# Kernel tuning notes

Hardware: AMD Instinct MI355X
Metric: run time of the kernel (lower is better)

The kernel has to match this reference:

```python
import math
import jax, jax.numpy as jnp
import numpy as np

R2PI = math.sqrt(2.0 * math.pi)


def setup_inputs() -> dict:
    key = jax.random.key(0)
    k1, k2, k3 = jax.random.split(key, 3)
    B, N, D = 16, 1024, 512
    feats = jax.random.normal(k1, (B, N, D), dtype=jnp.float32)
    ranges = jax.random.uniform(k2, (B, N), dtype=jnp.float32)  # Gaussian stddev per token
    durations = jax.random.randint(k3, (B, N), 1, 8, dtype=jnp.int64)
    # outlen is data-dependent in the torch code (.item()); fix it here as a static int
    outlen = int(jnp.max(jnp.sum(durations, axis=1)))
    return {"feats": feats, "ranges": ranges, "durations": durations, "outlen": outlen}


def reference(feats, ranges, durations, outlen):
    # feats: (B, N, D); ranges, durations: (B, N); outlen: static int
    dur = durations.astype(jnp.float32)
    # center per token (faithful to source: dur/2 + inclusive cumsum)
    c = dur / 2.0 + jnp.cumsum(dur, axis=1)            # (B, N)
    r = ranges + 1e-6                                   # (B, N)
    t = jnp.arange(outlen, dtype=jnp.float32)           # (T,)
    # z[b, t, n] = (t - c[b, n]) / r[b, n]
    z = (t[None, :, None] - c[:, None, :]) / r[:, None, :]          # (B, T, N)
    weights = jnp.exp(-0.5 * z * z) / (r[:, None, :] * R2PI) + 1e-6  # (B, T, N)
    weights = weights / jnp.sum(weights, axis=2, keepdims=True)
    # weighted sum of phoneme features per output frame
    return jnp.einsum("btn,bnd->btd", weights, feats)   # (B, T, D)
```

## Files before the change

kernel.cpp:

```cpp
#include <hip/hip_runtime.h>
#include <math.h>


#define B_ 16
#define N_ 1024
#define D_ 512
#define TB 8
#define MAXW 36
#define NCH 32

__global__ void scan_k(const int* __restrict__ dur, float* __restrict__ Q,
                       float* __restrict__ C) {
    int b = blockIdx.x;
    int lane = threadIdx.x;
    const int PER = N_ / 64;
    int base = b * N_ + lane * PER;
    int loc[PER];
    int s = 0;
#pragma unroll
    for (int i = 0; i < PER; ++i) { loc[i] = dur[base + i]; s += loc[i]; }
    int x = s;
#pragma unroll
    for (int off = 1; off < 64; off <<= 1) {
        int y = __shfl_up(x, off);
        if (lane >= off) x += y;
    }
    int run = x - s;
#pragma unroll
    for (int i = 0; i < PER; ++i) {
        Q[base + i] = (float)run;
        C[base + i] = (float)run + 1.5f * (float)loc[i];
        run += loc[i];
    }
}

__global__ void sumP_k(const float* __restrict__ feats, float* __restrict__ P) {
    int b = blockIdx.x;
    int ch = blockIdx.y;
    int tid = threadIdx.x;
    const float4* fb = (const float4*)(feats + ((size_t)b * N_ + (size_t)ch * 32) * D_);
    float4 a = make_float4(0.f, 0.f, 0.f, 0.f);
#pragma unroll 4
    for (int i = 0; i < 32; ++i) {
        float4 v = fb[(size_t)i * (D_ / 4) + tid];
        a.x += v.x; a.y += v.y; a.z += v.z; a.w += v.w;
    }
    ((float4*)(P + ((size_t)b * NCH + ch) * D_))[tid] = a;
}

__global__ void reduceS_k(const float* __restrict__ P, float* __restrict__ S) {
    int i = blockIdx.x * blockDim.x + threadIdx.x;
    if (i >= B_ * D_ / 4) return;
    int b = i / (D_ / 4);
    int d4 = i - b * (D_ / 4);
    const float4* p = (const float4*)P + (size_t)b * NCH * (D_ / 4) + d4;
    float4 a = make_float4(0.f, 0.f, 0.f, 0.f);
#pragma unroll
    for (int c = 0; c < NCH; ++c) {
        float4 v = p[(size_t)c * (D_ / 4)];
        a.x += v.x; a.y += v.y; a.z += v.z; a.w += v.w;
    }
    ((float4*)S)[i] = a;
}

__global__ __launch_bounds__(128) void upsample_k(
    const float* __restrict__ feats, const float* __restrict__ ranges,
    const float* __restrict__ Q, const float* __restrict__ C,
    const float* __restrict__ S, float* __restrict__ out, int T, int TG) {
    const int G = B_ * TG;
    int bid = blockIdx.x;
    int w = (bid & 7) * (G >> 3) + (bid >> 3);
    int b = w / TG;
    int tg = w - b * TG;
    int t0 = tg * TB;
    int tid = threadIdx.x;

    __shared__ float sg[MAXW][TB];

    const float* Qb = Q + b * N_;
    float loVal = (float)t0 - 18.5f;
    float hiVal = (float)t0 + (float)TB + 5.5f;
    int l = 0, r = N_;
    while (l < r) { int m = (l + r) >> 1; if (Qb[m] < loVal) l = m + 1; else r = m; }
    int lo = l;
    int l2 = lo, r2 = N_;
    while (l2 < r2) { int m = (l2 + r2) >> 1; if (Qb[m] <= hiVal) l2 = m + 1; else r2 = m; }
    int cnt = l2 - lo;
    if (cnt > MAXW) cnt = MAXW;

    if (tid < cnt) {
        int n = lo + tid;
        float rr = ranges[b * N_ + n] + 1e-6f;
        float inv = 1.0f / rr;
        float c = C[b * N_ + n];
        float base = inv * 0.3989422804014327f;
#pragma unroll
        for (int f = 0; f < TB; ++f) {
            float z = ((float)(t0 + f) - c) * inv;
            sg[tid][f] = base * __expf(-0.5f * z * z);
        }
    }
    __syncthreads();

    const float4* F = (const float4*)feats + (size_t)b * N_ * (D_ / 4) + tid;
    float4 acc[TB];
    float denom[TB];
#pragma unroll
    for (int f = 0; f < TB; ++f) {
        acc[f] = make_float4(0.f, 0.f, 0.f, 0.f);
        denom[f] = (float)N_ * 1e-6f;
    }
    for (int j = 0; j < cnt; ++j) {
        float4 fv = F[(size_t)(lo + j) * (D_ / 4)];
        float4 g0 = *(const float4*)&sg[j][0];
        float4 g1 = *(const float4*)&sg[j][4];
        denom[0] += g0.x; denom[1] += g0.y; denom[2] += g0.z; denom[3] += g0.w;
        denom[4] += g1.x; denom[5] += g1.y; denom[6] += g1.z; denom[7] += g1.w;
        float gg[TB] = {g0.x, g0.y, g0.z, g0.w, g1.x, g1.y, g1.z, g1.w};
#pragma unroll
        for (int f = 0; f < TB; ++f) {
            acc[f].x = fmaf(gg[f], fv.x, acc[f].x);
            acc[f].y = fmaf(gg[f], fv.y, acc[f].y);
            acc[f].z = fmaf(gg[f], fv.z, acc[f].z);
            acc[f].w = fmaf(gg[f], fv.w, acc[f].w);
        }
    }

    float4 s4 = ((const float4*)(S + b * D_))[tid];
#pragma unroll
    for (int f = 0; f < TB; ++f) {
        int t = t0 + f;
        if (t < T) {
            float inv = 1.0f / denom[f];
            float4 o;
            o.x = (acc[f].x + 1e-6f * s4.x) * inv;
            o.y = (acc[f].y + 1e-6f * s4.y) * inv;
            o.z = (acc[f].z + 1e-6f * s4.z) * inv;
            o.w = (acc[f].w + 1e-6f * s4.w) * inv;
            ((float4*)out)[((size_t)b * T + t) * (D_ / 4) + tid] = o;
        }
    }
}

extern "C" void kernel_launch(void* const* d_in, const int* in_sizes, int n_in,
                              void* d_out, int out_size, void* d_ws, size_t ws_size,
                              hipStream_t stream) {
    const float* feats  = (const float*)d_in[0];
    const float* ranges = (const float*)d_in[1];
    const int*   dur    = (const int*)d_in[2];
    float* out = (float*)d_out;
    int T = out_size / (B_ * D_);
    int TG = (T + TB - 1) / TB;

    float* Q = (float*)d_ws;
    float* C = Q + B_ * N_;
    float* S = C + B_ * N_;
    float* P = S + B_ * D_;

    scan_k<<<B_, 64, 0, stream>>>(dur, Q, C);
    dim3 gP(B_, NCH);
    sumP_k<<<gP, 128, 0, stream>>>(feats, P);
    reduceS_k<<<(B_ * D_ / 4 + 127) / 128, 128, 0, stream>>>(P, S);
    upsample_k<<<B_ * TG, 128, 0, stream>>>(feats, ranges, Q, C, S, out, T, TG);
}
```

Before: 177.5 us.

## Double frames per block and hoist normalizer sums into shared memory

Each block now computes 16 output frames instead of 8, so every feature row it loads is reused across twice as many frames. The shared window is widened to match the larger frame span. Gaussian weights are now computed cooperatively over (token, frame) pairs rather than one thread per token. Per-frame denominators are summed once by 16 threads and stored as reciprocals in shared memory, instead of every thread accumulating them redundantly. The trade-off is 64 float accumulators per thread, which raises register pressure, and half as many blocks.

```diff
diff --git a/kernel.cpp b/kernel.cpp
--- a/kernel.cpp
+++ b/kernel.cpp
@@ -5,8 +5,8 @@
 #define B_ 16
 #define N_ 1024
 #define D_ 512
-#define TB 8
-#define MAXW 36
+#define TB 16
+#define MAXW 44
 #define NCH 32
 
 __global__ void scan_k(const int* __restrict__ dur, float* __restrict__ Q,
@@ -76,6 +76,7 @@
     int tid = threadIdx.x;
 
     __shared__ float sg[MAXW][TB];
+    __shared__ float sinv[TB];
 
     const float* Qb = Q + b * N_;
     float loVal = (float)t0 - 18.5f;
@@ -88,42 +89,42 @@
     int cnt = l2 - lo;
     if (cnt > MAXW) cnt = MAXW;
 
-    if (tid < cnt) {
-        int n = lo + tid;
+    for (int idx = tid; idx < cnt * TB; idx += 128) {
+        int j = idx >> 4;
+        int f = idx & (TB - 1);
+        int n = lo + j;
         float rr = ranges[b * N_ + n] + 1e-6f;
         float inv = 1.0f / rr;
-        float c = C[b * N_ + n];
-        float base = inv * 0.3989422804014327f;
-#pragma unroll
-        for (int f = 0; f < TB; ++f) {
-            float z = ((float)(t0 + f) - c) * inv;
-            sg[tid][f] = base * __expf(-0.5f * z * z);
-        }
+        float z = ((float)(t0 + f) - C[b * N_ + n]) * inv;
+        sg[j][f] = 0.3989422804014327f * inv * __expf(-0.5f * z * z);
+    }
+    __syncthreads();
+    if (tid < TB) {
+        float dsum = (float)N_ * 1e-6f;
+        for (int j = 0; j < cnt; ++j) dsum += sg[j][tid];
+        sinv[tid] = 1.0f / dsum;
     }
     __syncthreads();
 
     const float4* F = (const float4*)feats + (size_t)b * N_ * (D_ / 4) + tid;
     float4 acc[TB];
-    float denom[TB];
 #pragma unroll
-    for (int f = 0; f < TB; ++f) {
-        acc[f] = make_float4(0.f, 0.f, 0.f, 0.f);
-        denom[f] = (float)N_ * 1e-6f;
-    }
+    for (int f = 0; f < TB; ++f) acc[f] = make_float4(0.f, 0.f, 0.f, 0.f);
+
     for (int j = 0; j < cnt; ++j) {
         float4 fv = F[(size_t)(lo + j) * (D_ / 4)];
-        float4 g0 = *(const float4*)&sg[j][0];
-        float4 g1 = *(const float4*)&sg[j][4];
-        denom[0] += g0.x; denom[1] += g0.y; denom[2] += g0.z; denom[3] += g0.w;
-        denom[4] += g1.x; denom[5] += g1.y; denom[6] += g1.z; denom[7] += g1.w;
-        float gg[TB] = {g0.x, g0.y, g0.z, g0.w, g1.x, g1.y, g1.z, g1.w};
-#pragma unroll
-        for (int f = 0; f < TB; ++f) {
-            acc[f].x = fmaf(gg[f], fv.x, acc[f].x);
-            acc[f].y = fmaf(gg[f], fv.y, acc[f].y);
-            acc[f].z = fmaf(gg[f], fv.z, acc[f].z);
-            acc[f].w = fmaf(gg[f], fv.w, acc[f].w);
-        }
+        const float4* gr = (const float4*)sg[j];
+        float4 g0 = gr[0], g1 = gr[1], g2 = gr[2], g3 = gr[3];
+#define ACC1(f, gv) \
+        acc[f].x = fmaf(gv, fv.x, acc[f].x); \
+        acc[f].y = fmaf(gv, fv.y, acc[f].y); \
+        acc[f].z = fmaf(gv, fv.z, acc[f].z); \
+        acc[f].w = fmaf(gv, fv.w, acc[f].w);
+        ACC1(0, g0.x)  ACC1(1, g0.y)  ACC1(2, g0.z)  ACC1(3, g0.w)
+        ACC1(4, g1.x)  ACC1(5, g1.y)  ACC1(6, g1.z)  ACC1(7, g1.w)
+        ACC1(8, g2.x)  ACC1(9, g2.y)  ACC1(10, g2.z) ACC1(11, g2.w)
+        ACC1(12, g3.x) ACC1(13, g3.y) ACC1(14, g3.z) ACC1(15, g3.w)
+#undef ACC1
     }
 
     float4 s4 = ((const float4*)(S + b * D_))[tid];
@@ -131,12 +132,12 @@
     for (int f = 0; f < TB; ++f) {
         int t = t0 + f;
         if (t < T) {
-            float inv = 1.0f / denom[f];
+            float si = sinv[f];
             float4 o;
-            o.x = (acc[f].x + 1e-6f * s4.x) * inv;
-            o.y = (acc[f].y + 1e-6f * s4.y) * inv;
-            o.z = (acc[f].z + 1e-6f * s4.z) * inv;
-            o.w = (acc[f].w + 1e-6f * s4.w) * inv;
+            o.x = (acc[f].x + 1e-6f * s4.x) * si;
+            o.y = (acc[f].y + 1e-6f * s4.y) * si;
+            o.z = (acc[f].z + 1e-6f * s4.z) * si;
+            o.w = (acc[f].w + 1e-6f * s4.w) * si;
             ((float4*)out)[((size_t)b * T + t) * (D_ / 4) + tid] = o;
         }
     }
```

Measured after the change: 177.3 us. About the same (-0.1%).
